# Optimization experiments

Measured on AMD Instinct MI355X. Metric: run time of the kernel, lower is better.

The kernel has to match this reference:

```python
import jax, jax.numpy as jnp
import numpy as np

H = 256      # hidden_size
B = 32       # batch
T = 4096     # timesteps / graph nodes
E = 8192     # edges per graph
PATH = 1
EXPAND_WEIGHT = 0.1
MODE = 'son'


def setup_inputs() -> dict:
    key = jax.random.key(0)
    ks = jax.random.split(key, 6)
    hidden = jax.random.normal(ks[0], (B, H), jnp.float32)
    encoder_outputs = jax.random.normal(ks[1], (T, B, H), jnp.float32)
    edges_src = jax.random.randint(ks[2], (B, E), 0, T)
    edges_dst = jax.random.randint(ks[3], (B, E), 0, T)
    # nn.Linear(2H, 2H) params (kaiming-uniform-ish scale) and the v vector
    lim = 1.0 / np.sqrt(2 * H)
    W_attn = jax.random.uniform(ks[4], (2 * H, 2 * H), jnp.float32, -lim, lim)
    b_attn = jnp.zeros((2 * H,), jnp.float32)
    v = jax.random.uniform(ks[5], (2 * H,), jnp.float32, -lim, lim)
    return {"hidden": hidden, "encoder_outputs": encoder_outputs,
            "edges_src": edges_src, "edges_dst": edges_dst,
            "W_attn": W_attn, "b_attn": b_attn, "v": v}


def reference(hidden, encoder_outputs, edges_src, edges_dst, W_attn, b_attn, v):
    Bb, Hh = hidden.shape
    Tt = encoder_outputs.shape[0]
    # h: [B, T, H] (hidden repeated over timesteps); enc: [B, T, H]
    h = jnp.broadcast_to(hidden[:, None, :], (Bb, Tt, Hh))
    enc = jnp.transpose(encoder_outputs, (1, 0, 2))
    # score: tanh(Linear(cat)) then v . energy -> [B, T]
    energy = jnp.tanh(jnp.concatenate([h, enc], axis=2) @ W_attn.T + b_attn)
    scores = jnp.einsum('btd,d->bt', energy, v)
    w = jax.nn.softmax(scores, axis=1)
    # expand_attn: scatter-add along graph edges, skipping consecutive (y == x+1)
    mask = (edges_dst != edges_src + 1).astype(w.dtype)  # [B, E]
    def scatter(wb, src, dst, m):
        if MODE == 'son':
            return jnp.zeros_like(wb).at[dst].add(wb[src] * m)
        else:
            return jnp.zeros_like(wb).at[src].add(wb[dst] * m)
    for _ in range(PATH):
        w = jax.vmap(scatter)(w, edges_src, edges_dst, mask) * EXPAND_WEIGHT
    return w[:, None, :]  # [B, 1, T]
```

## Files before the change

kernel.cpp:

```cpp
#include <hip/hip_runtime.h>
#include <hip/hip_bf16.h>

typedef __attribute__((ext_vector_type(8))) short bf16x8;
typedef __attribute__((ext_vector_type(4))) float f32x4;

#define HD 256
#define NB 32
#define NT 4096
#define NE 8192
#define N2 512
#define LDA 264

static __device__ __forceinline__ unsigned short f2bf(float f) {
  unsigned int u = __float_as_uint(f);
  u += 0x7fff + ((u >> 16) & 1);
  return (unsigned short)(u >> 16);
}

static __device__ __forceinline__ float fast_tanh(float x) {
  x = fminf(15.f, fmaxf(-15.f, x));
  float e = __expf(x + x);
  return (e - 1.f) * __builtin_amdgcn_rcpf(e + 1.f);
}

__global__ __launch_bounds__(256) void precompute_c(
    const float* __restrict__ hidden, const float* __restrict__ Wattn,
    const float* __restrict__ battn, float* __restrict__ cvec) {
  __shared__ float Ws[64 * 260];
  __shared__ float Hs[HD];
  const int tid = threadIdx.x;
  const int chunk = blockIdx.x & 7;
  const int b = blockIdx.x >> 3;
#pragma unroll
  for (int it = 0; it < 16; ++it) {
    int f = it * 1024 + tid * 4;
    int i = f >> 8, k = f & 255;
    float4 w4 = *(const float4*)(Wattn + (chunk * 64 + i) * N2 + k);
    *(float4*)&Ws[i * 260 + k] = w4;
  }
  if (tid < 64)
    *(float4*)&Hs[tid * 4] = *(const float4*)(hidden + b * HD + tid * 4);
  __syncthreads();
  const int nl = tid >> 2;
  const int kb = (tid & 3) * 64;
  float sum = 0.f;
#pragma unroll
  for (int z = 0; z < 64; z += 4) {
    float4 h4 = *(const float4*)&Hs[kb + z];
    float4 w4 = *(const float4*)&Ws[nl * 260 + kb + z];
    sum = fmaf(h4.x, w4.x, sum);
    sum = fmaf(h4.y, w4.y, sum);
    sum = fmaf(h4.z, w4.z, sum);
    sum = fmaf(h4.w, w4.w, sum);
  }
  sum += __shfl_xor(sum, 1, 64);
  sum += __shfl_xor(sum, 2, 64);
  if ((tid & 3) == 0)
    cvec[b * N2 + chunk * 64 + nl] = sum + battn[chunk * 64 + nl];
}

__global__ __launch_bounds__(256, 2) void score_gemm(
    const float* __restrict__ enc, const float* __restrict__ Wattn,
    const float* __restrict__ cvec, const float* __restrict__ vvec,
    float* __restrict__ scores) {
  __shared__ short As[64 * LDA];
  __shared__ short Bs[64 * LDA];
  __shared__ float part[2][64];
  const int tid = threadIdx.x;
  const int row0 = blockIdx.x * 64;
  const int w = tid >> 6;
  const int lane = tid & 63;
  const int q = lane >> 4;
  const int m = lane & 15;
  const int wr = 32 * (w >> 1);
  const int wc = 32 * (w & 1);

  {
    const float* src = enc + (long)row0 * HD;
#pragma unroll
    for (int it = 0; it < 16; ++it) {
      int f = it * 1024 + tid * 4;
      float4 a4 = *(const float4*)(src + f);
      int i = f >> 8, k = f & 255;
      *(short4*)&As[i * LDA + k] = make_short4(
          (short)f2bf(a4.x), (short)f2bf(a4.y), (short)f2bf(a4.z), (short)f2bf(a4.w));
    }
  }

  float rowacc[2][4] = {};

  for (int nt = 0; nt < 8; ++nt) {
    __syncthreads();
#pragma unroll
    for (int it = 0; it < 16; ++it) {
      int f = it * 1024 + tid * 4;
      int i = f >> 8, k = f & 255;
      float4 b4 = *(const float4*)(Wattn + (nt * 64 + i) * N2 + HD + k);
      *(short4*)&Bs[i * LDA + k] = make_short4(
          (short)f2bf(b4.x), (short)f2bf(b4.y), (short)f2bf(b4.z), (short)f2bf(b4.w));
    }
    __syncthreads();

    f32x4 acc00 = {}, acc01 = {}, acc10 = {}, acc11 = {};
#pragma unroll
    for (int kk = 0; kk < 8; ++kk) {
      const int ko = kk * 32 + q * 8;
      bf16x8 a0 = *(const bf16x8*)&As[(wr + m) * LDA + ko];
      bf16x8 a1 = *(const bf16x8*)&As[(wr + 16 + m) * LDA + ko];
      bf16x8 b0 = *(const bf16x8*)&Bs[(wc + m) * LDA + ko];
      bf16x8 b1 = *(const bf16x8*)&Bs[(wc + 16 + m) * LDA + ko];
      acc00 = __builtin_amdgcn_mfma_f32_16x16x32_bf16(a0, b0, acc00, 0, 0, 0);
      acc01 = __builtin_amdgcn_mfma_f32_16x16x32_bf16(a0, b1, acc01, 0, 0, 0);
      acc10 = __builtin_amdgcn_mfma_f32_16x16x32_bf16(a1, b0, acc10, 0, 0, 0);
      acc11 = __builtin_amdgcn_mfma_f32_16x16x32_bf16(a1, b1, acc11, 0, 0, 0);
    }

    const int n0 = nt * 64 + wc + m;
    const float v0 = vvec[n0];
    const float v1 = vvec[n0 + 16];
#pragma unroll
    for (int i = 0; i < 2; ++i) {
      const f32x4 ac0 = i ? acc10 : acc00;
      const f32x4 ac1 = i ? acc11 : acc01;
      float ej[4];
#pragma unroll
      for (int j = 0; j < 4; ++j) {
        const int bb = (wr + 16 * i + 4 * q + j) & 31;
        float e0 = fast_tanh(ac0[j] + cvec[bb * N2 + n0]);
        float e1 = fast_tanh(ac1[j] + cvec[bb * N2 + n0 + 16]);
        ej[j] = e0 * v0 + e1 * v1;
      }
#pragma unroll
      for (int j = 0; j < 4; ++j) {
        float sv = ej[j];
        sv += __shfl_xor(sv, 1, 64);
        sv += __shfl_xor(sv, 2, 64);
        sv += __shfl_xor(sv, 4, 64);
        sv += __shfl_xor(sv, 8, 64);
        rowacc[i][j] += sv;
      }
    }
  }

  if (m == 0) {
#pragma unroll
    for (int i = 0; i < 2; ++i)
#pragma unroll
      for (int j = 0; j < 4; ++j)
        part[w & 1][wr + 16 * i + 4 * q + j] = rowacc[i][j];
  }
  __syncthreads();
  if (tid < 64) {
    const int r = row0 + tid;
    scores[(r & 31) * NT + (r >> 5)] = part[0][tid] + part[1][tid];
  }
}

__global__ __launch_bounds__(1024) void softmax_scatter(
    float* __restrict__ w, const int* __restrict__ esrc,
    const int* __restrict__ edst) {
  __shared__ float wsv[NT];
  __shared__ float asv[NT];
  __shared__ float rtmp[16];
  __shared__ float rres;
  const int b = blockIdx.x;
  const int tid = threadIdx.x;
  const int wid = tid >> 6, lane = tid & 63;
  float s[4];
  float mx = -1e30f;
#pragma unroll
  for (int p = 0; p < 4; ++p) {
    s[p] = w[b * NT + tid + p * 1024];
    mx = fmaxf(mx, s[p]);
  }
#pragma unroll
  for (int d = 32; d >= 1; d >>= 1) mx = fmaxf(mx, __shfl_xor(mx, d, 64));
  if (lane == 0) rtmp[wid] = mx;
  __syncthreads();
  if (tid == 0) {
    float mm = rtmp[0];
#pragma unroll
    for (int i = 1; i < 16; ++i) mm = fmaxf(mm, rtmp[i]);
    rres = mm;
  }
  __syncthreads();
  mx = rres;
  float sm = 0.f;
#pragma unroll
  for (int p = 0; p < 4; ++p) {
    int i = tid + p * 1024;
    float e = __expf(s[p] - mx);
    wsv[i] = e;
    asv[i] = 0.f;
    sm += e;
  }
#pragma unroll
  for (int d = 32; d >= 1; d >>= 1) sm += __shfl_xor(sm, d, 64);
  if (lane == 0) rtmp[wid] = sm;
  __syncthreads();
  if (tid == 0) {
    float tt = 0.f;
#pragma unroll
    for (int i = 0; i < 16; ++i) tt += rtmp[i];
    rres = tt;
  }
  __syncthreads();
  const float inv = 1.0f / rres;

  for (int j = tid; j < NE; j += 1024) {
    int ss = esrc[b * NE + j];
    int dd = edst[b * NE + j];
    if (dd != ss + 1) atomicAdd(&asv[dd], wsv[ss]);
  }
  __syncthreads();
#pragma unroll
  for (int p = 0; p < 4; ++p) {
    int i = tid + p * 1024;
    w[b * NT + i] = 0.1f * asv[i] * inv;
  }
}

extern "C" void kernel_launch(void* const* d_in, const int* in_sizes, int n_in,
                              void* d_out, int out_size, void* d_ws, size_t ws_size,
                              hipStream_t stream) {
  const float* hidden = (const float*)d_in[0];
  const float* enc    = (const float*)d_in[1];
  const int*   esrc   = (const int*)d_in[2];
  const int*   edst   = (const int*)d_in[3];
  const float* Wattn  = (const float*)d_in[4];
  const float* battn  = (const float*)d_in[5];
  const float* vvec   = (const float*)d_in[6];
  float* out = (float*)d_out;
  float* cvec = (float*)d_ws;

  precompute_c<<<256, 256, 0, stream>>>(hidden, Wattn, battn, cvec);
  score_gemm<<<(NB * NT) / 64, 256, 0, stream>>>(enc, Wattn, cvec, vvec, out);
  softmax_scatter<<<NB, 1024, 0, stream>>>(out, esrc, edst);
}
```

Measured before the change: 311.7 us.

## Pre-convert W to bf16, hold B in registers, split softmax and scatter

A new prep kernel converts the encoder half of W_attn to bf16 once and writes the hidden projection transposed. The GEMM now uses 128-row tiles with an XOR-swizzled LDS A tile, and each wave keeps its bf16 weight fragments in registers across row tiles, so the repeated per-block W conversion and LDS staging go away. Softmax and the edge scatter become separate kernels, and the scatter uses global atomics spread over 512 blocks instead of 32. The costs are one extra launch, global atomic contention, and heavy register use per wave.

```diff
diff --git a/kernel.cpp b/kernel.cpp
--- a/kernel.cpp
+++ b/kernel.cpp
@@ -9,158 +9,144 @@
 #define NT 4096
 #define NE 8192
 #define N2 512
-#define LDA 264
 
 static __device__ __forceinline__ unsigned short f2bf(float f) {
   unsigned int u = __float_as_uint(f);
   u += 0x7fff + ((u >> 16) & 1);
   return (unsigned short)(u >> 16);
 }
-
+static __device__ __forceinline__ short4 cvt4(float4 a) {
+  return make_short4((short)f2bf(a.x), (short)f2bf(a.y),
+                     (short)f2bf(a.z), (short)f2bf(a.w));
+}
 static __device__ __forceinline__ float fast_tanh(float x) {
   x = fminf(15.f, fmaxf(-15.f, x));
   float e = __expf(x + x);
   return (e - 1.f) * __builtin_amdgcn_rcpf(e + 1.f);
 }
 
-__global__ __launch_bounds__(256) void precompute_c(
+__global__ __launch_bounds__(256) void prep(
     const float* __restrict__ hidden, const float* __restrict__ Wattn,
-    const float* __restrict__ battn, float* __restrict__ cvec) {
-  __shared__ float Ws[64 * 260];
-  __shared__ float Hs[HD];
+    const float* __restrict__ battn, float* __restrict__ cvecT,
+    short* __restrict__ Wbf) {
   const int tid = threadIdx.x;
-  const int chunk = blockIdx.x & 7;
-  const int b = blockIdx.x >> 3;
-#pragma unroll
-  for (int it = 0; it < 16; ++it) {
-    int f = it * 1024 + tid * 4;
-    int i = f >> 8, k = f & 255;
-    float4 w4 = *(const float4*)(Wattn + (chunk * 64 + i) * N2 + k);
-    *(float4*)&Ws[i * 260 + k] = w4;
-  }
-  if (tid < 64)
-    *(float4*)&Hs[tid * 4] = *(const float4*)(hidden + b * HD + tid * 4);
-  __syncthreads();
-  const int nl = tid >> 2;
-  const int kb = (tid & 3) * 64;
-  float sum = 0.f;
-#pragma unroll
-  for (int z = 0; z < 64; z += 4) {
-    float4 h4 = *(const float4*)&Hs[kb + z];
-    float4 w4 = *(const float4*)&Ws[nl * 260 + kb + z];
-    sum = fmaf(h4.x, w4.x, sum);
-    sum = fmaf(h4.y, w4.y, sum);
-    sum = fmaf(h4.z, w4.z, sum);
-    sum = fmaf(h4.w, w4.w, sum);
-  }
-  sum += __shfl_xor(sum, 1, 64);
-  sum += __shfl_xor(sum, 2, 64);
-  if ((tid & 3) == 0)
-    cvec[b * N2 + chunk * 64 + nl] = sum + battn[chunk * 64 + nl];
-}
-
-__global__ __launch_bounds__(256, 2) void score_gemm(
-    const float* __restrict__ enc, const float* __restrict__ Wattn,
-    const float* __restrict__ cvec, const float* __restrict__ vvec,
-    float* __restrict__ scores) {
-  __shared__ short As[64 * LDA];
-  __shared__ short Bs[64 * LDA];
-  __shared__ float part[2][64];
-  const int tid = threadIdx.x;
-  const int row0 = blockIdx.x * 64;
-  const int w = tid >> 6;
-  const int lane = tid & 63;
-  const int q = lane >> 4;
-  const int m = lane & 15;
-  const int wr = 32 * (w >> 1);
-  const int wc = 32 * (w & 1);
-
-  {
-    const float* src = enc + (long)row0 * HD;
-#pragma unroll
-    for (int it = 0; it < 16; ++it) {
-      int f = it * 1024 + tid * 4;
-      float4 a4 = *(const float4*)(src + f);
-      int i = f >> 8, k = f & 255;
-      *(short4*)&As[i * LDA + k] = make_short4(
-          (short)f2bf(a4.x), (short)f2bf(a4.y), (short)f2bf(a4.z), (short)f2bf(a4.w));
-    }
-  }
-
-  float rowacc[2][4] = {};
-
-  for (int nt = 0; nt < 8; ++nt) {
-    __syncthreads();
+  if (blockIdx.x < 256) {
+    __shared__ float Ws[64 * 260];
+    __shared__ float Hs[HD];
+    const int chunk = blockIdx.x & 7;
+    const int b = blockIdx.x >> 3;
 #pragma unroll
     for (int it = 0; it < 16; ++it) {
       int f = it * 1024 + tid * 4;
       int i = f >> 8, k = f & 255;
-      float4 b4 = *(const float4*)(Wattn + (nt * 64 + i) * N2 + HD + k);
-      *(short4*)&Bs[i * LDA + k] = make_short4(
-          (short)f2bf(b4.x), (short)f2bf(b4.y), (short)f2bf(b4.z), (short)f2bf(b4.w));
-    }
+      float4 w4 = *(const float4*)(Wattn + (chunk * 64 + i) * N2 + k);
+      *(float4*)&Ws[i * 260 + k] = w4;
+    }
+    if (tid < 64)
+      *(float4*)&Hs[tid * 4] = *(const float4*)(hidden + b * HD + tid * 4);
     __syncthreads();
-
-    f32x4 acc00 = {}, acc01 = {}, acc10 = {}, acc11 = {};
-#pragma unroll
-    for (int kk = 0; kk < 8; ++kk) {
-      const int ko = kk * 32 + q * 8;
-      bf16x8 a0 = *(const bf16x8*)&As[(wr + m) * LDA + ko];
-      bf16x8 a1 = *(const bf16x8*)&As[(wr + 16 + m) * LDA + ko];
-      bf16x8 b0 = *(const bf16x8*)&Bs[(wc + m) * LDA + ko];
-      bf16x8 b1 = *(const bf16x8*)&Bs[(wc + 16 + m) * LDA + ko];
-      acc00 = __builtin_amdgcn_mfma_f32_16x16x32_bf16(a0, b0, acc00, 0, 0, 0);
-      acc01 = __builtin_amdgcn_mfma_f32_16x16x32_bf16(a0, b1, acc01, 0, 0, 0);
-      acc10 = __builtin_amdgcn_mfma_f32_16x16x32_bf16(a1, b0, acc10, 0, 0, 0);
-      acc11 = __builtin_amdgcn_mfma_f32_16x16x32_bf16(a1, b1, acc11, 0, 0, 0);
-    }
-
-    const int n0 = nt * 64 + wc + m;
-    const float v0 = vvec[n0];
-    const float v1 = vvec[n0 + 16];
-#pragma unroll
-    for (int i = 0; i < 2; ++i) {
-      const f32x4 ac0 = i ? acc10 : acc00;
-      const f32x4 ac1 = i ? acc11 : acc01;
-      float ej[4];
+    const int nl = tid >> 2;
+    const int kb = (tid & 3) * 64;
+    float sum = 0.f;
+#pragma unroll
+    for (int z = 0; z < 64; z += 4) {
+      float4 h4 = *(const float4*)&Hs[kb + z];
+      float4 w4 = *(const float4*)&Ws[nl * 260 + kb + z];
+      sum = fmaf(h4.x, w4.x, sum);
+      sum = fmaf(h4.y, w4.y, sum);
+      sum = fmaf(h4.z, w4.z, sum);
+      sum = fmaf(h4.w, w4.w, sum);
+    }
+    sum += __shfl_xor(sum, 1, 64);
+    sum += __shfl_xor(sum, 2, 64);
+    if ((tid & 3) == 0)
+      cvecT[(chunk * 64 + nl) * NB + b] = sum + battn[chunk * 64 + nl];
+  } else {
+    int f = (blockIdx.x - 256) * 1024 + tid * 4;
+    int n = f >> 8, k = f & 255;
+    float4 w4 = *(const float4*)(Wattn + n * N2 + HD + k);
+    *(short4*)(Wbf + f) = cvt4(w4);
+  }
+}
+
+__global__ __launch_bounds__(256, 2) void score_gemm(
+    const float* __restrict__ enc, const short* __restrict__ Wbf,
+    const float* __restrict__ cvecT, const float* __restrict__ vvec,
+    float* __restrict__ scores) {
+  __shared__ short As[128 * 256];
+  __shared__ float part[4][128];
+  const int tid = threadIdx.x;
+  const int w = tid >> 6, lane = tid & 63, q = lane >> 4, m = lane & 15;
+  const long row0 = (long)blockIdx.x * 128;
+
+  ((float*)part)[tid] = 0.f;
+  ((float*)part)[tid + 256] = 0.f;
+
+  const float* src = enc + row0 * HD;
+#pragma unroll
+  for (int it = 0; it < 32; ++it) {
+    int f = it * 1024 + tid * 4;
+    float4 a4 = *(const float4*)(src + f);
+    int r = f >> 8, k = f & 255;
+    int slot = (k >> 3) ^ (r & 31);
+    *(short4*)&As[(r * 32 + slot) * 8 + (k & 7)] = cvt4(a4);
+  }
+  __syncthreads();
+
+#pragma unroll 1
+  for (int cc = 0; cc < 2; ++cc) {
+    const int nb = cc * 256 + w * 64;
+    bf16x8 breg[4][8];
+    float vv[4];
+    float4 cv[4][2];
+#pragma unroll
+    for (int c = 0; c < 4; ++c) {
+      const int n = nb + c * 16 + m;
+      const short* bp = Wbf + n * HD + q * 8;
+#pragma unroll
+      for (int kk = 0; kk < 8; ++kk) breg[c][kk] = *(const bf16x8*)(bp + kk * 32);
+      vv[c] = vvec[n];
+      cv[c][0] = *(const float4*)(cvecT + n * NB + q * 4);
+      cv[c][1] = *(const float4*)(cvecT + n * NB + 16 + q * 4);
+    }
+#pragma unroll 1
+    for (int rt = 0; rt < 8; ++rt) {
+      const int r = rt * 16 + m;
+      const int rx = r & 31;
+      f32x4 acc[4] = {{0.f,0.f,0.f,0.f},{0.f,0.f,0.f,0.f},
+                      {0.f,0.f,0.f,0.f},{0.f,0.f,0.f,0.f}};
+#pragma unroll
+      for (int kk = 0; kk < 8; ++kk) {
+        bf16x8 a = *(const bf16x8*)&As[(r * 32 + ((kk * 4 + q) ^ rx)) * 8];
+#pragma unroll
+        for (int c = 0; c < 4; ++c)
+          acc[c] = __builtin_amdgcn_mfma_f32_16x16x32_bf16(a, breg[c][kk], acc[c], 0, 0, 0);
+      }
+      const int p = rt & 1;
 #pragma unroll
       for (int j = 0; j < 4; ++j) {
-        const int bb = (wr + 16 * i + 4 * q + j) & 31;
-        float e0 = fast_tanh(ac0[j] + cvec[bb * N2 + n0]);
-        float e1 = fast_tanh(ac1[j] + cvec[bb * N2 + n0 + 16]);
-        ej[j] = e0 * v0 + e1 * v1;
+        float e = fast_tanh(acc[0][j] + cv[0][p][j]) * vv[0]
+                + fast_tanh(acc[1][j] + cv[1][p][j]) * vv[1]
+                + fast_tanh(acc[2][j] + cv[2][p][j]) * vv[2]
+                + fast_tanh(acc[3][j] + cv[3][p][j]) * vv[3];
+        e += __shfl_xor(e, 1, 64);
+        e += __shfl_xor(e, 2, 64);
+        e += __shfl_xor(e, 4, 64);
+        e += __shfl_xor(e, 8, 64);
+        if (m == 0) part[w][rt * 16 + 4 * q + j] += e;
       }
-#pragma unroll
-      for (int j = 0; j < 4; ++j) {
-        float sv = ej[j];
-        sv += __shfl_xor(sv, 1, 64);
-        sv += __shfl_xor(sv, 2, 64);
-        sv += __shfl_xor(sv, 4, 64);
-        sv += __shfl_xor(sv, 8, 64);
-        rowacc[i][j] += sv;
-      }
-    }
-  }
-
-  if (m == 0) {
-#pragma unroll
-    for (int i = 0; i < 2; ++i)
-#pragma unroll
-      for (int j = 0; j < 4; ++j)
-        part[w & 1][wr + 16 * i + 4 * q + j] = rowacc[i][j];
-  }
-  __syncthreads();
-  if (tid < 64) {
-    const int r = row0 + tid;
-    scores[(r & 31) * NT + (r >> 5)] = part[0][tid] + part[1][tid];
-  }
-}
-
-__global__ __launch_bounds__(1024) void softmax_scatter(
-    float* __restrict__ w, const int* __restrict__ esrc,
-    const int* __restrict__ edst) {
-  __shared__ float wsv[NT];
-  __shared__ float asv[NT];
+    }
+  }
+  __syncthreads();
+  if (tid < 128) {
+    const long r = row0 + tid;
+    scores[(r & 31) * NT + (r >> 5)] =
+        part[0][tid] + part[1][tid] + part[2][tid] + part[3][tid];
+  }
+}
+
+__global__ __launch_bounds__(1024) void softmax_norm(
+    float* __restrict__ sc, float* __restrict__ out) {
   __shared__ float rtmp[16];
   __shared__ float rres;
   const int b = blockIdx.x;
@@ -170,7 +156,7 @@
   float mx = -1e30f;
 #pragma unroll
   for (int p = 0; p < 4; ++p) {
-    s[p] = w[b * NT + tid + p * 1024];
+    s[p] = sc[b * NT + tid + p * 1024];
     mx = fmaxf(mx, s[p]);
   }
 #pragma unroll
@@ -188,11 +174,8 @@
   float sm = 0.f;
 #pragma unroll
   for (int p = 0; p < 4; ++p) {
-    int i = tid + p * 1024;
-    float e = __expf(s[p] - mx);
-    wsv[i] = e;
-    asv[i] = 0.f;
-    sm += e;
+    s[p] = __expf(s[p] - mx);
+    sm += s[p];
   }
 #pragma unroll
   for (int d = 32; d >= 1; d >>= 1) sm += __shfl_xor(sm, d, 64);
@@ -205,19 +188,23 @@
     rres = tt;
   }
   __syncthreads();
-  const float inv = 1.0f / rres;
-
-  for (int j = tid; j < NE; j += 1024) {
-    int ss = esrc[b * NE + j];
-    int dd = edst[b * NE + j];
-    if (dd != ss + 1) atomicAdd(&asv[dd], wsv[ss]);
-  }
-  __syncthreads();
+  const float scale = 0.1f / rres;
 #pragma unroll
   for (int p = 0; p < 4; ++p) {
     int i = tid + p * 1024;
-    w[b * NT + i] = 0.1f * asv[i] * inv;
-  }
+    sc[b * NT + i] = s[p] * scale;
+    out[b * NT + i] = 0.f;
+  }
+}
+
+__global__ __launch_bounds__(512) void scatter(
+    const float* __restrict__ wn, const int* __restrict__ esrc,
+    const int* __restrict__ edst, float* __restrict__ out) {
+  const int b = blockIdx.x >> 4;
+  const int e = (blockIdx.x & 15) * 512 + threadIdx.x;
+  const int ss = esrc[b * NE + e];
+  const int dd = edst[b * NE + e];
+  if (dd != ss + 1) atomicAdd(out + b * NT + dd, wn[b * NT + ss]);
 }
 
 extern "C" void kernel_launch(void* const* d_in, const int* in_sizes, int n_in,
@@ -231,9 +218,14 @@
   const float* battn  = (const float*)d_in[5];
   const float* vvec   = (const float*)d_in[6];
   float* out = (float*)d_out;
-  float* cvec = (float*)d_ws;
-
-  precompute_c<<<256, 256, 0, stream>>>(hidden, Wattn, battn, cvec);
-  score_gemm<<<(NB * NT) / 64, 256, 0, stream>>>(enc, Wattn, cvec, vvec, out);
-  softmax_scatter<<<NB, 1024, 0, stream>>>(out, esrc, edst);
-}
+
+  char* ws = (char*)d_ws;
+  float* cvecT  = (float*)ws;
+  short* Wbf    = (short*)(ws + 65536);
+  float* scores = (float*)(ws + 65536 + 262144);
+
+  prep<<<384, 256, 0, stream>>>(hidden, Wattn, battn, cvecT, Wbf);
+  score_gemm<<<(NB * NT) / 128, 256, 0, stream>>>(enc, Wbf, cvecT, vvec, scores);
+  softmax_norm<<<NB, 1024, 0, stream>>>(scores, out);
+  scatter<<<512, 512, 0, stream>>>(scores, esrc, edst, out);
+}
```

New measurement: 319.5 us. +2.5%, slower.
